# Kernel tuning notes

Measured on AMD Instinct MI355X. Metric: run time of the kernel, lower is better.

The kernel has to match this reference:

```python
import jax, jax.numpy as jnp
import numpy as np

_BASE = [[15,13],[13,11],[16,14],[14,12],[11,12],[5,11],[6,12],[5,6],[5,7],[6,8],[7,9],[8,10],[1,2],[0,1],[0,2],[1,3],[2,4],[3,5],[4,6]]
_CONN_NP = np.array(_BASE + [[b, a] for a, b in _BASE], dtype=np.int64).T  # [2, 38]: row0=src, row1=dst
N_NODES = 17
_ADJ_NP = np.zeros((N_NODES, N_NODES), dtype=bool)
_ADJ_NP[_CONN_NP[1], _CONN_NP[0]] = True   # message flows src -> dst: mask[dst, src]
np.fill_diagonal(_ADJ_NP, True)            # PyG GATConv add_self_loops=True default
ADJ = jnp.asarray(_ADJ_NP)
CONN = jnp.asarray(_CONN_NP)

B, T, NUM_CLASSES, HEADS = 128, 24, 500, 8
LSTM_H = 512
FEAT = N_NODES * 256 + 256  # 4608
NEG_INF = -1e9


def _gat_layer(x, W, a_src, a_dst, b, concat):
    # x: [G, 17, Cin]; W: [Cin, H*D]; a_src/a_dst: [H, D]; dense attention over tiny 17-node graph
    G, N, _ = x.shape
    H, D = a_src.shape
    h = (x @ W).reshape(G, N, H, D)
    s_src = jnp.einsum('gnhd,hd->gnh', h, a_src)
    s_dst = jnp.einsum('gnhd,hd->gnh', h, a_dst)
    e = jax.nn.leaky_relu(s_dst[:, :, None, :] + s_src[:, None, :, :], 0.2)  # [G, i_dst, j_src, H]
    e = jnp.where(ADJ[None, :, :, None], e, NEG_INF)
    alpha = jax.nn.softmax(e, axis=2)  # softmax over incoming neighbors j (incl. self loop)
    out = jnp.einsum('gijh,gjhd->gihd', alpha, h)
    out = out.reshape(G, N, H * D) if concat else out.mean(axis=2)
    return out + b


def _edge_feats(pose_flat):  # [G, 17, 3] -> [G, 38, 2] (bone lengths + angles)
    v = pose_flat[:, CONN[1], :2] - pose_flat[:, CONN[0], :2]
    lengths = jnp.linalg.norm(v, axis=-1)
    angles = jnp.arctan2(v[..., 1], v[..., 0])
    return jnp.stack([lengths, angles], axis=-1)


def _lstm_dir(x, Wih, Whh, bih, bhh):
    # x: [N, T, F] -> h sequence [N, T, H]; torch gate order i, f, g, o
    Hsz = Whh.shape[1]
    n = x.shape[0]
    def step(carry, xt):
        h, c = carry
        g = xt @ Wih.T + h @ Whh.T + bih + bhh
        i, f, gg, o = jnp.split(g, 4, axis=-1)
        c = jax.nn.sigmoid(f) * c + jax.nn.sigmoid(i) * jnp.tanh(gg)
        h = jax.nn.sigmoid(o) * jnp.tanh(c)
        return (h, c), h
    init = (jnp.zeros((n, Hsz), x.dtype), jnp.zeros((n, Hsz), x.dtype))
    _, hs = jax.lax.scan(step, init, jnp.swapaxes(x, 0, 1))
    return jnp.swapaxes(hs, 0, 1)


def _forward(pose1, pose2, W1, as1, ad1, b1, W2, as2, ad2, b2, W3, as3, ad3, b3,
             fc_w, fc_b, bn_g, bn_b, bn_mean, bn_var,
             Wih_f, Whh_f, bih_f, bhh_f, Wih_b, Whh_b, bih_b, bhh_b, cls_w, cls_b):
    def run(pose):
        x = pose.reshape(-1, N_NODES, 3)  # [B*T, 17, 3], all timestep graphs batched
        x = jax.nn.elu(_gat_layer(x, W1, as1, ad1, b1, True))   # [G,17,512]
        x = jax.nn.elu(_gat_layer(x, W2, as2, ad2, b2, True))   # [G,17,1024]
        x = _gat_layer(x, W3, as3, ad3, b3, False)              # [G,17,256]
        g = x.reshape(B, T, N_NODES * 256)
        ef = _edge_feats(pose.reshape(-1, N_NODES, 3)).reshape(-1, 38) @ fc_w + fc_b
        return jnp.concatenate([g, ef.reshape(B, T, -1)], axis=-1)  # [B,T,4608]
    comb = jnp.concatenate([run(pose1), run(pose2)], axis=0)  # modal==0 path: [2B,24,4608]
    # BatchNorm1d(24) in eval mode: normalize the time-channel axis with running stats
    comb = (comb - bn_mean[None, :, None]) * (bn_g[None, :, None] / jnp.sqrt(bn_var[None, :, None] + 1e-5)) + bn_b[None, :, None]
    hf = _lstm_dir(comb, Wih_f, Whh_f, bih_f, bhh_f)
    hb = jnp.flip(_lstm_dir(jnp.flip(comb, 1), Wih_b, Whh_b, bih_b, bhh_b), 1)
    lstm_out = jnp.concatenate([hf, hb], axis=-1)[:, -1, :]  # [2B, 1024]
    return lstm_out, lstm_out @ cls_w + cls_b


def setup_inputs():
    key = jax.random.key(0)
    ks = jax.random.split(key, 20)
    def w(k, shape):
        fan_in = shape[0] if len(shape) == 2 else shape[-1]
        return (jax.random.normal(k, shape, jnp.float32) / jnp.sqrt(jnp.float32(fan_in)))
    return {
        'pose1': jax.random.normal(ks[0], (B, T, N_NODES, 3), jnp.float32),
        'pose2': jax.random.normal(ks[1], (B, T, N_NODES, 3), jnp.float32),
        'modal': 0,
        'W1': w(ks[2], (3, HEADS * 64)), 'as1': w(ks[3], (HEADS, 64)), 'ad1': w(ks[4], (HEADS, 64)), 'b1': jnp.zeros((HEADS * 64,), jnp.float32),
        'W2': w(ks[5], (HEADS * 64, HEADS * 128)), 'as2': w(ks[6], (HEADS, 128)), 'ad2': w(ks[7], (HEADS, 128)), 'b2': jnp.zeros((HEADS * 128,), jnp.float32),
        'W3': w(ks[8], (HEADS * 128, HEADS * 256)), 'as3': w(ks[9], (HEADS, 256)), 'ad3': w(ks[10], (HEADS, 256)), 'b3': jnp.zeros((256,), jnp.float32),
        'fc_w': w(ks[11], (38, 128)), 'fc_b': jnp.zeros((128,), jnp.float32),
        'bn_g': jnp.ones((T,), jnp.float32), 'bn_b': jnp.zeros((T,), jnp.float32),
        'bn_mean': jnp.zeros((T,), jnp.float32), 'bn_var': jnp.ones((T,), jnp.float32),
        'Wih_f': w(ks[12], (4 * LSTM_H, FEAT)), 'Whh_f': w(ks[13], (4 * LSTM_H, LSTM_H)),
        'bih_f': jnp.zeros((4 * LSTM_H,), jnp.float32), 'bhh_f': jnp.zeros((4 * LSTM_H,), jnp.float32),
        'Wih_b': w(ks[14], (4 * LSTM_H, FEAT)), 'Whh_b': w(ks[15], (4 * LSTM_H, LSTM_H)),
        'bih_b': jnp.zeros((4 * LSTM_H,), jnp.float32), 'bhh_b': jnp.zeros((4 * LSTM_H,), jnp.float32),
        'cls_w': w(ks[16], (2 * LSTM_H, NUM_CLASSES)), 'cls_b': jnp.zeros((NUM_CLASSES,), jnp.float32),
    }


def reference(pose1, pose2, modal, W1, as1, ad1, b1, W2, as2, ad2, b2, W3, as3, ad3, b3,
              fc_w, fc_b, bn_g, bn_b, bn_mean, bn_var,
              Wih_f, Whh_f, bih_f, bhh_f, Wih_b, Whh_b, bih_b, bhh_b, cls_w, cls_b):
    # modal==0 path of the original forward (both modalities)
    return _forward(pose1, pose2, W1, as1, ad1, b1, W2, as2, ad2, b2, W3, as3, ad3, b3,
                    fc_w, fc_b, bn_g, bn_b, bn_mean, bn_var,
                    Wih_f, Whh_f, bih_f, bhh_f, Wih_b, Whh_b, bih_b, bhh_b, cls_w, cls_b)
```

## Files before the change

### kernel.cpp

```cpp
#include <hip/hip_runtime.h>
#include <hip/hip_bf16.h>

typedef __hip_bfloat16 bf16;
typedef short short8 __attribute__((ext_vector_type(8)));
typedef __bf16 bf16x8 __attribute__((ext_vector_type(8)));
typedef float f32x4 __attribute__((ext_vector_type(4)));
typedef const __attribute__((address_space(1))) void* gas_t;
typedef __attribute__((address_space(3))) void* las_t;

__constant__ unsigned int ADJM[17] = {
  0x00007u,0x0000Fu,0x00017u,0x0002Au,0x00054u,0x008E8u,0x01170u,0x002A0u,
  0x00540u,0x00280u,0x00500u,0x03820u,0x05840u,0x0A800u,0x15000u,0x0A000u,0x14000u};

__constant__ int EA[38] = {15,13,16,14,11,5,6,5,5,6,7,8,1,0,0,1,2,3,4,
                           13,11,14,12,12,11,12,6,7,8,9,10,2,1,2,3,4,5,6};
__constant__ int EB[38] = {13,11,14,12,12,11,12,6,7,8,9,10,2,1,2,3,4,5,6,
                           15,13,16,14,11,5,6,5,5,6,7,8,1,0,0,1,2,3,4};

__device__ __forceinline__ float b2f(bf16 v){ return __bfloat162float(v); }
__device__ __forceinline__ bf16 f2b(float v){ return __float2bfloat16(v); }
__device__ __forceinline__ float s2f(short s){
  unsigned u = ((unsigned)(unsigned short)s) << 16;
  float f; __builtin_memcpy(&f, &u, 4); return f;
}
__device__ __forceinline__ float ldx(const void* p, size_t i, int ext){
  return ext ? ((const float*)p)[i] : b2f(((const bf16*)p)[i]);
}
__device__ __forceinline__ void stx(void* p, size_t i, int ext, float v){
  if (ext) ((float*)p)[i] = v;
  else     ((bf16*)p)[i] = f2b(v);
}
__device__ __forceinline__ float sigm(float x){ return 1.f/(1.f + expf(-x)); }

__global__ void detect_k(const void* probe, int* flag){
  if (blockIdx.x == 0 && threadIdx.x == 0) {
    const bf16* p = (const bf16*)probe;
    int ext = 0;
    for (int i = 0; i < 256; i++) {
      float v = b2f(p[i]);
      if (!(fabsf(v) < 1e6f)) ext = 1;
    }
    *flag = ext;
  }
}

__global__ __launch_bounds__(256) void conv_k(
    const void* __restrict__ in, bf16* __restrict__ out, long n,
    const int* __restrict__ flg){
  int ext = *flg;
  long i = (long)blockIdx.x * 256 + threadIdx.x;
  if (i < n) out[i] = f2b(ldx(in, i, ext));
}

__global__ __launch_bounds__(256) void transp_k(
    const void* __restrict__ in, bf16* __restrict__ out, int K, int N,
    const int* __restrict__ flg){
  int ext = *flg;
  __shared__ float t[32][33];
  int k0 = blockIdx.y * 32, n0 = blockIdx.x * 32;
  int c = threadIdx.x & 31, r8 = threadIdx.x >> 5;
  for (int rr = r8; rr < 32; rr += 8) {
    int k = k0 + rr, n = n0 + c;
    t[rr][c] = (k < K && n < N) ? ldx(in, (size_t)k*N + n, ext) : 0.f;
  }
  __syncthreads();
  for (int rr = r8; rr < 32; rr += 8) {
    int n = n0 + rr, k = k0 + c;
    if (n < N && k < K) out[(size_t)n*K + k] = f2b(t[c][rr]);
  }
}

__global__ __launch_bounds__(256) void posepad_k(
    const void* __restrict__ pose1, const void* __restrict__ pose2,
    bf16* __restrict__ P32, const int* __restrict__ flg){
  int ext = *flg;
  long i = (long)blockIdx.x * 256 + threadIdx.x;
  if (i >= (long)6144*17*32) return;
  int col = i & 31; long rn = i >> 5;
  int n = (int)(rn % 17); long g = rn / 17;
  float v = 0.f;
  if (col < 3) {
    int pose = g >= 3072 ? 1 : 0;
    long gp = g - (pose ? 3072 : 0);
    v = ldx(pose ? pose2 : pose1, gp*51 + n*3 + col, ext);
  }
  P32[i] = f2b(v);
}

__global__ __launch_bounds__(256) void w1pad_k(
    const void* __restrict__ W1, bf16* __restrict__ W1p,
    const int* __restrict__ flg){
  int ext = *flg;
  int i = blockIdx.x * 256 + threadIdx.x;
  if (i >= 512*32) return;
  int col = i & 31, n = i >> 5;
  W1p[i] = f2b(col < 3 ? ldx(W1, (size_t)col*512 + n, ext) : 0.f);
}

__global__ __launch_bounds__(256) void smallprep_k(
    const void* s0, const void* s1, const void* s2, const void* s3,
    const void* s4, const void* s5, const void* s6, const void* s7,
    const void* s8, const void* s9, const void* s10,
    const void* bng, const void* bnb, const void* bnm, const void* bnv,
    bf16* __restrict__ sml, const int* __restrict__ flg)
{
  int ext = *flg;
  if (blockIdx.x == 55) {
    int t = threadIdx.x;
    if (t < 24) {
      float sc = ldx(bng, t, ext) * rsqrtf(ldx(bnv, t, ext) + 1e-5f);
      float sh = ldx(bnb, t, ext) - ldx(bnm, t, ext) * sc;
      sml[14080 + t] = f2b(sc);
      sml[14112 + t] = f2b(sh);
    }
    return;
  }
  long gidx = (long)blockIdx.x*256 + threadIdx.x;
  if (gidx >= 13952) return;
  const void* srcs[11] = {s0,s1,s2,s3,s4,s5,s6,s7,s8,s9,s10};
  const int lens[11] = {512,512,512,1024,1024,1024,2048,2048,256,4864,128};
  int seg = 0; long off = gidx;
  while (off >= lens[seg]) { off -= lens[seg]; seg++; }
  sml[gidx] = f2b(ldx(srcs[seg], off, ext));
}

__global__ __launch_bounds__(256) void gemm_mfma(
    const bf16* __restrict__ A, long lda,
    const bf16* __restrict__ Bt, long ldb,
    void* __restrict__ Cout, long ldc, int outF32,
    const float* __restrict__ addsrc, long ldadd,
    const void* __restrict__ bias0, const void* __restrict__ bias1,
    int M, int N, int K, const int* __restrict__ flg)
{
  __shared__ short lsA[128*32];
  __shared__ short lsB[128*32];
  int tid = threadIdx.x;
  int lane = tid & 63, w = tid >> 6;
  int wm = (w >> 1) * 64, wn = (w & 1) * 64;
  int lr = lane & 15;
  int lk = (lane >> 4) * 8;
  int m0 = blockIdx.y * 128, n0 = blockIdx.x * 128;
  const short* Ag = (const short*)A;
  const short* Bg = (const short*)Bt;
  int rowS = tid >> 2;
  int kqS  = (tid & 3) * 8;

  f32x4 acc[4][4];
#pragma unroll
  for (int i = 0; i < 4; i++)
#pragma unroll
    for (int j = 0; j < 4; j++) acc[i][j] = (f32x4)0.f;

  for (int kb = 0; kb < K; kb += 32) {
#pragma unroll
    for (int s = 0; s < 2; s++) {
      int row = s*64 + rowS;
      const short* ga = Ag + (size_t)(m0+row)*lda + kb + kqS;
      const short* gb = Bg + (size_t)(n0+row)*ldb + kb + kqS;
      __builtin_amdgcn_global_load_lds((gas_t)ga, (las_t)(lsA + s*2048 + w*512), 16, 0, 0);
      __builtin_amdgcn_global_load_lds((gas_t)gb, (las_t)(lsB + s*2048 + w*512), 16, 0, 0);
    }
    __syncthreads();
    bf16x8 af[4], bfr[4];
#pragma unroll
    for (int i = 0; i < 4; i++)
      af[i] = *(bf16x8*)&lsA[(wm + i*16 + lr)*32 + lk];
#pragma unroll
    for (int j = 0; j < 4; j++)
      bfr[j] = *(bf16x8*)&lsB[(wn + j*16 + lr)*32 + lk];
#pragma unroll
    for (int i = 0; i < 4; i++)
#pragma unroll
      for (int j = 0; j < 4; j++)
        acc[i][j] = __builtin_amdgcn_mfma_f32_16x16x32_bf16(af[i], bfr[j], acc[i][j], 0, 0, 0);
    __syncthreads();
  }

  int ext = flg ? *flg : 0;
#pragma unroll
  for (int j = 0; j < 4; j++) {
    int col = n0 + wn + j*16 + (lane & 15);
    float bsum = 0.f;
    if (bias0) bsum += ldx(bias0, col, ext);
    if (bias1) bsum += ldx(bias1, col, ext);
#pragma unroll
    for (int i = 0; i < 4; i++) {
      int rowb = m0 + wm + i*16 + (lane >> 4)*4;
#pragma unroll
      for (int r = 0; r < 4; r++) {
        float v = acc[i][j][r] + bsum;
        int row = rowb + r;
        if (addsrc) v += addsrc[(size_t)row*ldadd + col];
        size_t ci = (size_t)row*ldc + col;
        if (outF32) ((float*)Cout)[ci] = v;
        else        ((bf16*)Cout)[ci] = f2b(v);
      }
    }
  }
}

__global__ __launch_bounds__(256) void gemm_k(
    const void* __restrict__ A, long aOff, long lda, int aMode,
    const void* __restrict__ B, long ldb, int bT, int bExt,
    void* __restrict__ Cout, long outOff, long ldc, int outMode,
    const float* __restrict__ addsrc, long ldadd,
    const void* __restrict__ bias0, const void* __restrict__ bias1,
    int M, int N, int K, const int* __restrict__ flg)
{
  int ext  = *flg;
  int aF32 = (aMode == 1) || (aMode == 2 && ext);
  int bF32 = (bExt && ext);
  int oF32 = (outMode == 1) || (outMode == 2 && ext);

  __shared__ float As[16][64];
  __shared__ float Bs[16][64];
  int tid = threadIdx.x;
  int tx = tid & 15, ty = tid >> 4;
  int m0 = blockIdx.y * 64, n0 = blockIdx.x * 64;
  float acc[4][4] = {};

  for (int kb = 0; kb < K; kb += 16) {
#pragma unroll
    for (int i = 0; i < 4; i++) {
      int idx = i*256 + tid;
      int m = idx & 63, k = idx >> 6;
      int gm = m0 + m, gk = kb + k;
      float v = 0.f;
      if (gm < M && gk < K) {
        size_t ai = (size_t)aOff + (size_t)gm*lda + gk;
        v = aF32 ? ((const float*)A)[ai] : b2f(((const bf16*)A)[ai]);
      }
      As[k][m] = v;
    }
#pragma unroll
    for (int i = 0; i < 4; i++) {
      int idx = i*256 + tid;
      int n = idx & 63, k = idx >> 6;
      int gn = n0 + n, gk = kb + k;
      float v = 0.f;
      if (gn < N && gk < K) {
        size_t bi = bT ? (size_t)gn*ldb + gk : (size_t)gk*ldb + gn;
        v = bF32 ? ((const float*)B)[bi] : b2f(((const bf16*)B)[bi]);
      }
      Bs[k][n] = v;
    }
    __syncthreads();
#pragma unroll
    for (int kk = 0; kk < 16; kk++) {
      float a[4], b[4];
#pragma unroll
      for (int i = 0; i < 4; i++) a[i] = As[kk][ty*4 + i];
#pragma unroll
      for (int j = 0; j < 4; j++) b[j] = Bs[kk][tx*4 + j];
#pragma unroll
      for (int i = 0; i < 4; i++)
#pragma unroll
        for (int j = 0; j < 4; j++)
          acc[i][j] = fmaf(a[i], b[j], acc[i][j]);
    }
    __syncthreads();
  }

#pragma unroll
  for (int i = 0; i < 4; i++) {
    int gm = m0 + ty*4 + i;
    if (gm >= M) continue;
#pragma unroll
    for (int j = 0; j < 4; j++) {
      int gn = n0 + tx*4 + j;
      if (gn >= N) continue;
      float v = acc[i][j];
      if (bias0)  v += ldx(bias0, gn, ext);
      if (bias1)  v += ldx(bias1, gn, ext);
      if (addsrc) v += addsrc[(size_t)gm*ldadd + gn];
      size_t ci = (size_t)outOff + (size_t)gm*ldc + gn;
      if (oF32) ((float*)Cout)[ci] = v;
      else      ((bf16*)Cout)[ci] = f2b(v);
    }
  }
}

__global__ __launch_bounds__(256) void scoremax_k(
    const bf16* __restrict__ H,
    const bf16* __restrict__ aS, const bf16* __restrict__ aD,
    float* __restrict__ alphaG, int D, int HD)
{
  __shared__ float sS[17][8], sD_[17][8];
  int g = blockIdx.x, tid = threadIdx.x;
  int lane = tid & 63, w = tid >> 6;
  int cpl = HD >> 6;
  int col0 = lane * cpl;
  int h = lane >> 3;
  const short* Hgs = (const short*)(H + (size_t)g*17*HD);
  const short* a0 = (const short*)aS;
  const short* a1 = (const short*)aD;

  for (int n = w; n < 17; n += 4) {
    float s0 = 0.f, s1 = 0.f;
    const short* hp = Hgs + (size_t)n*HD + col0;
    for (int z = 0; z < cpl; z += 8) {
      short8 hv = *(const short8*)&hp[z];
      short8 v0 = *(const short8*)&a0[col0 + z];
      short8 v1 = *(const short8*)&a1[col0 + z];
#pragma unroll
      for (int e = 0; e < 8; e++) {
        float hf = s2f(hv[e]);
        s0 = fmaf(hf, s2f(v0[e]), s0);
        s1 = fmaf(hf, s2f(v1[e]), s1);
      }
    }
#pragma unroll
    for (int off = 1; off < 8; off <<= 1) {
      s0 += __shfl_xor(s0, off);
      s1 += __shfl_xor(s1, off);
    }
    if ((lane & 7) == 0) { sS[n][h] = s0; sD_[n][h] = s1; }
  }
  __syncthreads();

  if (tid < 136) {
    int i = tid >> 3, hh = tid & 7;
    unsigned int msk = ADJM[i];
    float e[17], m = -1e30f;
    for (int j = 0; j < 17; j++)
      if ((msk >> j) & 1u) {
        float v = sD_[i][hh] + sS[j][hh];
        v = v > 0.f ? v : 0.2f * v;
        e[j] = v;
        if (v > m) m = v;
      }
    float sum = 0.f;
    float wv[17];
    for (int j = 0; j < 17; j++) {
      float wj = 0.f;
      if ((msk >> j) & 1u) { wj = expf(e[j] - m); sum += wj; }
      wv[j] = wj;
    }
    float inv = 1.f / sum;
    float* ag = alphaG + (size_t)g*2312;
    for (int j = 0; j < 17; j++)
      ag[(i*17 + j)*8 + hh] = wv[j] * inv;
  }
}

__global__ __launch_bounds__(256) void agg_k(
    const bf16* __restrict__ H, const float* __restrict__ alphaG,
    const bf16* __restrict__ bias,
    bf16* __restrict__ Xout, bf16* __restrict__ comb,
    const bf16* __restrict__ bnsc_, const bf16* __restrict__ bnsh_,
    int D, int HD, int meanMode, int chunkStart)
{
  __shared__ float al[2312];
  int g = blockIdx.x, tid = threadIdx.x;
  for (int v = tid; v < 2312; v += 256) al[v] = alphaG[(size_t)g*2312 + v];
  __syncthreads();
  const short* Hgs = (const short*)(H + (size_t)g*17*HD);

  if (!meanMode) {
    int nc = HD >> 8;
    for (int cc = 0; cc < nc; cc++) {
      int c = cc*256 + tid;
      int h = c / D;
      float Hreg[17];
#pragma unroll
      for (int j = 0; j < 17; j++) Hreg[j] = s2f(Hgs[(size_t)j*HD + c]);
      float b0 = b2f(bias[c]);
      for (int i = 0; i < 17; i++) {
        float acc = b0;
#pragma unroll
        for (int j = 0; j < 17; j++)
          acc = fmaf(al[(i*17 + j)*8 + h], Hreg[j], acc);
        float v = acc > 0.f ? acc : expm1f(acc);
        Xout[((size_t)g*17 + i)*HD + c] = f2b(v);
      }
    }
  } else {
    float acc[17];
#pragma unroll
    for (int i = 0; i < 17; i++) acc[i] = 0.f;
    for (int hh = 0; hh < 8; hh++) {
      float Hreg[17];
#pragma unroll
      for (int j = 0; j < 17; j++)
        Hreg[j] = s2f(Hgs[(size_t)j*2048 + hh*256 + tid]);
      for (int i = 0; i < 17; i++) {
        float a = acc[i];
#pragma unroll
        for (int j = 0; j < 17; j++)
          a = fmaf(al[(i*17 + j)*8 + hh], Hreg[j], a);
        acc[i] = a;
      }
    }
    int gg = chunkStart + g;
    int pose = gg >= 3072 ? 1 : 0;
    int gp = gg - pose*3072;
    int bb = gp / 24, t = gp - bb*24;
    int r = (pose*128 + bb)*24 + t;
    float sc = b2f(bnsc_[t]);
    float sh = b2f(bnsh_[t]);
    float b0 = b2f(bias[tid]);
#pragma unroll
    for (int i = 0; i < 17; i++) {
      float v = acc[i] * 0.125f + b0;
      comb[(size_t)r*4608 + i*256 + tid] = f2b(v * sc + sh);
    }
  }
}

__global__ __launch_bounds__(256) void ef_k(
    const void* __restrict__ pose1, const void* __restrict__ pose2,
    const bf16* __restrict__ fcw, const bf16* __restrict__ fcb,
    bf16* __restrict__ comb,
    const bf16* __restrict__ bnsc_, const bf16* __restrict__ bnsh_,
    const int* __restrict__ flg)
{
  int ext = *flg;
  int g = blockIdx.x;
  int pose = g >= 3072 ? 1 : 0;
  int gp = g - pose*3072;
  const void* P = pose ? pose2 : pose1;
  size_t base = (size_t)gp * 51;
  __shared__ float feat[76];
  int tid = threadIdx.x;
  if (tid < 38) {
    int a = EA[tid], b = EB[tid];
    float ax = ldx(P, base + a*3+0, ext), ay = ldx(P, base + a*3+1, ext);
    float bx = ldx(P, base + b*3+0, ext), by = ldx(P, base + b*3+1, ext);
    float vx = bx - ax, vy = by - ay;
    feat[2*tid]   = sqrtf(vx*vx + vy*vy);
    feat[2*tid+1] = atan2f(vy, vx);
  }
  __syncthreads();
  int bb = gp / 24, t = gp - bb*24;
  int r = (pose*128 + bb)*24 + t;
  float sc = b2f(bnsc_[t]), sh = b2f(bnsh_[t]);
  int row = tid >> 7, c = tid & 127;
  float acc = b2f(fcb[c]);
  for (int k = 0; k < 38; k++)
    acc = fmaf(feat[row*38 + k], b2f(fcw[k*128 + c]), acc);
  comb[(size_t)r*4608 + 4352 + row*128 + c] = f2b(acc * sc + sh);
}

__global__ __launch_bounds__(256) void lstm_point(
    const float* __restrict__ gates, long gstride,
    const float* __restrict__ cprev,
    float* __restrict__ cout_, float* __restrict__ hout,
    bf16* __restrict__ h16,
    void* __restrict__ dout, float* __restrict__ fout, int doff,
    const int* __restrict__ flg)
{
  int ext = *flg;
  int idx = blockIdx.x * 256 + threadIdx.x;
  if (idx >= 256*512) return;
  int n = idx >> 9, u = idx & 511;
  const float* gp = gates + (size_t)n * gstride;
  float gi = gp[u], gf = gp[512+u], gc = gp[1024+u], go = gp[1536+u];
  float cp = cprev ? cprev[idx] : 0.f;
  float c = sigm(gf)*cp + sigm(gi)*tanhf(gc);
  float h = sigm(go)*tanhf(c);
  cout_[idx] = c;
  if (hout) hout[idx] = h;
  if (h16) h16[idx] = f2b(h);
  if (dout) stx(dout, (size_t)n*1024 + doff + u, ext, h);
  if (fout) fout[(size_t)n*1024 + doff + u] = h;
}

extern "C" void kernel_launch(void* const* d_in, const int* in_sizes, int n_in,
                              void* d_out, int out_size, void* d_ws, size_t ws_size,
                              hipStream_t stream)
{
  const void* pose1 = d_in[0];
  const void* pose2 = d_in[1];
  int wb = (n_in == 30) ? 2 : 3;
  const void* W1  = d_in[wb+0];
  const void* as1 = d_in[wb+1];
  const void* ad1 = d_in[wb+2];
  const void* b1  = d_in[wb+3];
  const void* W2  = d_in[wb+4];
  const void* as2 = d_in[wb+5];
  const void* ad2 = d_in[wb+6];
  const void* b2  = d_in[wb+7];
  const void* W3  = d_in[wb+8];
  const void* as3 = d_in[wb+9];
  const void* ad3 = d_in[wb+10];
  const void* b3  = d_in[wb+11];
  const void* fcw = d_in[wb+12];
  const void* fcb = d_in[wb+13];
  const void* bng = d_in[wb+14];
  const void* bnb = d_in[wb+15];
  const void* bnm = d_in[wb+16];
  const void* bnv = d_in[wb+17];
  const void* Wih_f = d_in[wb+18];
  const void* Whh_f = d_in[wb+19];
  const void* bih_f = d_in[wb+20];
  const void* bhh_f = d_in[wb+21];
  const void* Wih_b = d_in[wb+22];
  const void* Whh_b = d_in[wb+23];
  const void* bih_b = d_in[wb+24];
  const void* bhh_b = d_in[wb+25];
  const void* cls_w = d_in[wb+26];
  const void* cls_b = d_in[wb+27];
  (void)Whh_b;

  auto al = [](size_t x){ return (x + 255) & ~(size_t)255; };
  size_t flagB  = 256;
  size_t combB  = al((size_t)6144*4608*2);
  size_t gatesB_ = al((size_t)256*2048*4);
  size_t gatesBB = al((size_t)256*2048*4);
  size_t cB     = al((size_t)256*512*4);
  size_t h16B   = al((size_t)256*512*2);
  size_t l32B   = al((size_t)256*1024*4);
  size_t w2tB   = al((size_t)1024*512*2);
  size_t w3tB   = al((size_t)2048*1024*2);
  size_t whhB   = al((size_t)2048*512*2);
  size_t wihB   = al((size_t)2048*4608*2);
  size_t p32B   = al((size_t)6144*17*32*2);
  size_t w1pB   = al((size_t)512*32*2);
  size_t smlB   = al((size_t)32768*2);
  size_t xifB   = al((size_t)6144*2048*4);
  size_t fixB   = flagB + combB + gatesB_ + gatesBB + cB + h16B + l32B
                + w2tB + w3tB + whhB + 2*wihB + p32B + w1pB + smlB;
  auto chunkB = [&](int C){
    return al((size_t)C*17*2048*2) + al((size_t)C*17*1024*2)
         + al((size_t)C*2312*4);
  };
  const int cands[8] = {3072,1536,768,384,192,96,48,24};
  int CHUNK = 0; bool useXIf = false;
  for (int i = 0; i < 8 && !CHUNK; i++)
    if (fixB + xifB + chunkB(cands[i]) <= ws_size) { CHUNK = cands[i]; useXIf = true; }
  for (int i = 0; i < 8 && !CHUNK; i++)
    if (fixB + chunkB(cands[i]) <= ws_size) CHUNK = cands[i];
  if (!CHUNK) CHUNK = 24;

  char* ws = (char*)d_ws;
  size_t off = 0;
  auto alloc = [&](size_t bytes) -> void* { void* p = ws + off; off += bytes; return p; };
  int*   dflag  = (int*)  alloc(flagB);
  bf16*  comb   = (bf16*) alloc(combB);
  float* gates  = (float*)alloc(gatesB_);
  float* gatesBw= (float*)alloc(gatesBB);
  float* cbuf   = (float*)alloc(cB);
  bf16*  h16    = (bf16*) alloc(h16B);
  float* lstm32 = (float*)alloc(l32B);
  bf16*  W2t    = (bf16*) alloc(w2tB);
  bf16*  W3t    = (bf16*) alloc(w3tB);
  bf16*  WhhC   = (bf16*) alloc(whhB);
  bf16*  WihfC  = (bf16*) alloc(wihB);
  bf16*  WihbC  = (bf16*) alloc(wihB);
  bf16*  P32    = (bf16*) alloc(p32B);
  bf16*  W1p    = (bf16*) alloc(w1pB);
  bf16*  sml    = (bf16*) alloc(smlB);
  float* XIf    = useXIf ? (float*)alloc(xifB) : nullptr;
  bf16*  Hbuf   = (bf16*) alloc(al((size_t)CHUNK*17*2048*2));
  bf16*  Xbuf   = (bf16*) alloc(al((size_t)CHUNK*17*1024*2));
  float* alphaA = (float*)alloc(al((size_t)CHUNK*2312*4));

  bf16* as1c = sml;          bf16* ad1c = sml + 512;
  bf16* b1c  = sml + 1024;   bf16* as2c = sml + 1536;
  bf16* ad2c = sml + 2560;   bf16* b2c  = sml + 3584;
  bf16* as3c = sml + 4608;   bf16* ad3c = sml + 6656;
  bf16* b3c  = sml + 8704;   bf16* fcwc = sml + 8960;
  bf16* fcbc = sml + 13824;  bf16* bnsc = sml + 14080;
  bf16* bnsh = sml + 14112;

  int RPC = CHUNK * 17;
  int gy  = (RPC + 63) / 64;
  int nchunks = 6144 / CHUNK;
  bool mfmaGat = (RPC % 128) == 0;
  dim3 blk(256);

  detect_k<<<dim3(1), dim3(64), 0, stream>>>(pose1, dflag);

  long nWih = (long)2048*4608;
  conv_k<<<dim3((unsigned)((nWih+255)/256)), blk, 0, stream>>>(Wih_f, WihfC, nWih, dflag);
  conv_k<<<dim3((unsigned)((nWih+255)/256)), blk, 0, stream>>>(Wih_b, WihbC, nWih, dflag);
  long nWhh = (long)2048*512;
  conv_k<<<dim3((unsigned)((nWhh+255)/256)), blk, 0, stream>>>(Whh_f, WhhC, nWhh, dflag);
  transp_k<<<dim3(1024/32, 512/32), blk, 0, stream>>>(W2, W2t, 512, 1024, dflag);
  transp_k<<<dim3(2048/32, 1024/32), blk, 0, stream>>>(W3, W3t, 1024, 2048, dflag);
  posepad_k<<<dim3((unsigned)(((long)6144*17*32+255)/256)), blk, 0, stream>>>(pose1, pose2, P32, dflag);
  w1pad_k<<<dim3(64), blk, 0, stream>>>(W1, W1p, dflag);
  smallprep_k<<<dim3(56), blk, 0, stream>>>(
      as1, ad1, b1, as2, ad2, b2, as3, ad3, b3, fcw, fcb,
      bng, bnb, bnm, bnv, sml, dflag);

  for (int c = 0; c < nchunks; c++) {
    int cstart = c * CHUNK;
    if (mfmaGat)
      gemm_mfma<<<dim3(512/128, RPC/128), blk, 0, stream>>>(
          P32 + (size_t)cstart*17*32, 32L, W1p, 32L, Hbuf, 512L, 0,
          (const float*)nullptr, 0L, nullptr, nullptr, RPC, 512, 32, dflag);
    else {
      int pose   = cstart / 3072;
      long pOff  = (long)(cstart % 3072) * 51;
      gemm_k<<<dim3(512/64, gy), blk, 0, stream>>>(
          pose ? pose2 : pose1, pOff, 3L, 2, W1, 512L, 0, 1, Hbuf, 0L, 512L, 0,
          (const float*)nullptr, 0L, (const void*)nullptr, (const void*)nullptr,
          RPC, 512, 3, dflag);
    }
    scoremax_k<<<dim3(CHUNK), blk, 0, stream>>>(Hbuf, as1c, ad1c, alphaA, 64, 512);
    agg_k<<<dim3(CHUNK), blk, 0, stream>>>(
        Hbuf, alphaA, b1c, Xbuf, (bf16*)nullptr,
        (const bf16*)nullptr, (const bf16*)nullptr, 64, 512, 0, 0);
    if (mfmaGat)
      gemm_mfma<<<dim3(1024/128, RPC/128), blk, 0, stream>>>(
          Xbuf, 512L, W2t, 512L, Hbuf, 1024L, 0,
          (const float*)nullptr, 0L, nullptr, nullptr, RPC, 1024, 512, dflag);
    else
      gemm_k<<<dim3(1024/64, gy), blk, 0, stream>>>(
          Xbuf, 0L, 512L, 0, W2t, 512L, 1, 0, Hbuf, 0L, 1024L, 0,
          (const float*)nullptr, 0L, (const void*)nullptr, (const void*)nullptr,
          RPC, 1024, 512, dflag);
    scoremax_k<<<dim3(CHUNK), blk, 0, stream>>>(Hbuf, as2c, ad2c, alphaA, 128, 1024);
    agg_k<<<dim3(CHUNK), blk, 0, stream>>>(
        Hbuf, alphaA, b2c, Xbuf, (bf16*)nullptr,
        (const bf16*)nullptr, (const bf16*)nullptr, 128, 1024, 0, 0);
    if (mfmaGat)
      gemm_mfma<<<dim3(2048/128, RPC/128), blk, 0, stream>>>(
          Xbuf, 1024L, W3t, 1024L, Hbuf, 2048L, 0,
          (const float*)nullptr, 0L, nullptr, nullptr, RPC, 2048, 1024, dflag);
    else
      gemm_k<<<dim3(2048/64, gy), blk, 0, stream>>>(
          Xbuf, 0L, 1024L, 0, W3t, 1024L, 1, 0, Hbuf, 0L, 2048L, 0,
          (const float*)nullptr, 0L, (const void*)nullptr, (const void*)nullptr,
          RPC, 2048, 1024, dflag);
    scoremax_k<<<dim3(CHUNK), blk, 0, stream>>>(Hbuf, as3c, ad3c, alphaA, 256, 2048);
    agg_k<<<dim3(CHUNK), blk, 0, stream>>>(
        Hbuf, alphaA, b3c, (bf16*)nullptr, comb,
        bnsc, bnsh, 256, 2048, 1, cstart);
  }

  ef_k<<<dim3(6144), blk, 0, stream>>>(pose1, pose2, fcwc, fcbc, comb,
                                       bnsc, bnsh, dflag);

  gemm_mfma<<<dim3(2048/128, 256/128), blk, 0, stream>>>(
      comb + (size_t)23*4608, (long)24*4608, WihbC, 4608L, gatesBw, 2048L, 1,
      (const float*)nullptr, 0L, bih_b, bhh_b, 256, 2048, 4608, dflag);

  if (useXIf) {
    gemm_mfma<<<dim3(2048/128, 6144/128), blk, 0, stream>>>(
        comb, 4608L, WihfC, 4608L, XIf, 2048L, 1,
        (const float*)nullptr, 0L, bih_f, bhh_f, 6144, 2048, 4608, dflag);
    lstm_point<<<dim3(512), blk, 0, stream>>>(
        XIf, (long)24*2048, (const float*)nullptr, cbuf, (float*)nullptr, h16,
        (void*)nullptr, (float*)nullptr, 0, dflag);
    for (int t = 1; t < 24; t++) {
      gemm_mfma<<<dim3(2048/128, 256/128), blk, 0, stream>>>(
          h16, 512L, WhhC, 512L, gates, 2048L, 1,
          XIf + (size_t)t*2048, (long)24*2048,
          nullptr, nullptr, 256, 2048, 512, dflag);
      lstm_point<<<dim3(512), blk, 0, stream>>>(
          gates, 2048L, cbuf, cbuf, (float*)nullptr, h16,
          (t == 23) ? d_out : (void*)nullptr,
          (t == 23) ? lstm32 : (float*)nullptr, 0, dflag);
    }
  } else {
    for (int t = 0; t < 24; t++) {
      gemm_mfma<<<dim3(2048/128, 256/128), blk, 0, stream>>>(
          comb + (size_t)t*4608, (long)24*4608, WihfC, 4608L, gates, 2048L, 1,
          (const float*)nullptr, 0L, bih_f, bhh_f, 256, 2048, 4608, dflag);
      if (t > 0)
        gemm_mfma<<<dim3(2048/128, 256/128), blk, 0, stream>>>(
            h16, 512L, WhhC, 512L, gates, 2048L, 1,
            gates, 2048L, nullptr, nullptr, 256, 2048, 512, dflag);
      lstm_point<<<dim3(512), blk, 0, stream>>>(
          gates, 2048L, (t == 0) ? (const float*)nullptr : cbuf, cbuf,
          (float*)nullptr, h16,
          (t == 23) ? d_out : (void*)nullptr,
          (t == 23) ? lstm32 : (float*)nullptr, 0, dflag);
    }
  }

  lstm_point<<<dim3(512), blk, 0, stream>>>(
      gatesBw, 2048L, (const float*)nullptr, cbuf, (float*)nullptr,
      (bf16*)nullptr, d_out, lstm32, 512, dflag);

  gemm_k<<<dim3((500+63)/64, 256/64), blk, 0, stream>>>(
      lstm32, 0L, 1024L, 1, cls_w, 500L, 0, 1, d_out, 262144L, 500L, 2,
      (const float*)nullptr, 0L, cls_b, (const void*)nullptr, 256, 500, 1024, dflag);
}
```

Measured before the change: 3.562 ms.

## Fuse GAT score/aggregate kernels and LSTM recurrent GEMM with pointwise update

Merges the GAT attention-score and aggregation kernels into one kernel that keeps the attention weights in shared memory, removing the global alpha buffer round trip and one launch per layer. The LSTM weights are reordered so the four gates of each unit sit next to each other. That lets a new per-step kernel do the h·Whh MFMA and the cell update together, with ping-pong h buffers and pre-summed biases. This halves launches in the 24-step recurrence and removes the gates round trip through global memory. The cost is a small 64x64 tile grid (128 blocks) for the recurrent GEMM, which may leave much of the GPU idle.

After: 2.993 ms. 1.19x faster.

```diff
diff --git a/kernel.cpp b/kernel.cpp
--- a/kernel.cpp
+++ b/kernel.cpp
@@ -44,12 +44,27 @@
   }
 }
 
-__global__ __launch_bounds__(256) void conv_k(
-    const void* __restrict__ in, bf16* __restrict__ out, long n,
+__global__ __launch_bounds__(256) void reord_k(
+    const void* __restrict__ in, bf16* __restrict__ out, int K,
     const int* __restrict__ flg){
   int ext = *flg;
   long i = (long)blockIdx.x * 256 + threadIdx.x;
-  if (i < n) out[i] = f2b(ldx(in, i, ext));
+  if (i >= (long)2048*K) return;
+  long rowp = i / K, k = i - rowp*K;
+  int u = (int)(rowp >> 2), g = (int)(rowp & 3);
+  out[i] = f2b(ldx(in, (size_t)(g*512 + u)*K + k, ext));
+}
+
+__global__ __launch_bounds__(256) void biasprep_k(
+    const void* bihf, const void* bhhf, const void* bihb, const void* bhhb,
+    float* __restrict__ bIf, float* __restrict__ bIb,
+    const int* __restrict__ flg){
+  int ext = *flg;
+  int c = blockIdx.x*256 + threadIdx.x;
+  if (c >= 2048) return;
+  int u = c >> 2, g = c & 3;
+  bIf[c] = ldx(bihf, (size_t)g*512+u, ext) + ldx(bhhf, (size_t)g*512+u, ext);
+  bIb[c] = ldx(bihb, (size_t)g*512+u, ext) + ldx(bhhb, (size_t)g*512+u, ext);
 }
 
 __global__ __launch_bounds__(256) void transp_k(
@@ -280,41 +295,47 @@
   }
 }
 
-__global__ __launch_bounds__(256) void scoremax_k(
+__global__ __launch_bounds__(256) void attn_k(
     const bf16* __restrict__ H,
     const bf16* __restrict__ aS, const bf16* __restrict__ aD,
-    float* __restrict__ alphaG, int D, int HD)
+    const bf16* __restrict__ bias,
+    bf16* __restrict__ Xout, bf16* __restrict__ comb,
+    const bf16* __restrict__ bnsc_, const bf16* __restrict__ bnsh_,
+    int D, int HD, int meanMode, int chunkStart)
 {
   __shared__ float sS[17][8], sD_[17][8];
+  __shared__ float al[2312];
   int g = blockIdx.x, tid = threadIdx.x;
   int lane = tid & 63, w = tid >> 6;
-  int cpl = HD >> 6;
-  int col0 = lane * cpl;
-  int h = lane >> 3;
   const short* Hgs = (const short*)(H + (size_t)g*17*HD);
-  const short* a0 = (const short*)aS;
-  const short* a1 = (const short*)aD;
-
-  for (int n = w; n < 17; n += 4) {
-    float s0 = 0.f, s1 = 0.f;
-    const short* hp = Hgs + (size_t)n*HD + col0;
-    for (int z = 0; z < cpl; z += 8) {
-      short8 hv = *(const short8*)&hp[z];
-      short8 v0 = *(const short8*)&a0[col0 + z];
-      short8 v1 = *(const short8*)&a1[col0 + z];
-#pragma unroll
-      for (int e = 0; e < 8; e++) {
-        float hf = s2f(hv[e]);
-        s0 = fmaf(hf, s2f(v0[e]), s0);
-        s1 = fmaf(hf, s2f(v1[e]), s1);
-      }
-    }
-#pragma unroll
-    for (int off = 1; off < 8; off <<= 1) {
-      s0 += __shfl_xor(s0, off);
-      s1 += __shfl_xor(s1, off);
-    }
-    if ((lane & 7) == 0) { sS[n][h] = s0; sD_[n][h] = s1; }
+
+  {
+    int cpl = HD >> 6;
+    int col0 = lane * cpl;
+    int h = lane >> 3;
+    const short* a0 = (const short*)aS;
+    const short* a1 = (const short*)aD;
+    for (int n = w; n < 17; n += 4) {
+      float s0 = 0.f, s1 = 0.f;
+      const short* hp = Hgs + (size_t)n*HD + col0;
+      for (int z = 0; z < cpl; z += 8) {
+        short8 hv = *(const short8*)&hp[z];
+        short8 v0 = *(const short8*)&a0[col0 + z];
+        short8 v1 = *(const short8*)&a1[col0 + z];
+#pragma unroll
+        for (int e = 0; e < 8; e++) {
+          float hf = s2f(hv[e]);
+          s0 = fmaf(hf, s2f(v0[e]), s0);
+          s1 = fmaf(hf, s2f(v1[e]), s1);
+        }
+      }
+#pragma unroll
+      for (int off = 1; off < 8; off <<= 1) {
+        s0 += __shfl_xor(s0, off);
+        s1 += __shfl_xor(s1, off);
+      }
+      if ((lane & 7) == 0) { sS[n][h] = s0; sD_[n][h] = s1; }
+    }
   }
   __syncthreads();
 
@@ -329,32 +350,16 @@
         e[j] = v;
         if (v > m) m = v;
       }
-    float sum = 0.f;
-    float wv[17];
+    float sum = 0.f, wv[17];
     for (int j = 0; j < 17; j++) {
       float wj = 0.f;
       if ((msk >> j) & 1u) { wj = expf(e[j] - m); sum += wj; }
       wv[j] = wj;
     }
     float inv = 1.f / sum;
-    float* ag = alphaG + (size_t)g*2312;
-    for (int j = 0; j < 17; j++)
-      ag[(i*17 + j)*8 + hh] = wv[j] * inv;
-  }
-}
-
-__global__ __launch_bounds__(256) void agg_k(
-    const bf16* __restrict__ H, const float* __restrict__ alphaG,
-    const bf16* __restrict__ bias,
-    bf16* __restrict__ Xout, bf16* __restrict__ comb,
-    const bf16* __restrict__ bnsc_, const bf16* __restrict__ bnsh_,
-    int D, int HD, int meanMode, int chunkStart)
-{
-  __shared__ float al[2312];
-  int g = blockIdx.x, tid = threadIdx.x;
-  for (int v = tid; v < 2312; v += 256) al[v] = alphaG[(size_t)g*2312 + v];
+    for (int j = 0; j < 17; j++) al[(i*17 + j)*8 + hh] = wv[j] * inv;
+  }
   __syncthreads();
-  const short* Hgs = (const short*)(H + (size_t)g*17*HD);
 
   if (!meanMode) {
     int nc = HD >> 8;
@@ -441,28 +446,95 @@
   comb[(size_t)r*4608 + 4352 + row*128 + c] = f2b(acc * sc + sh);
 }
 
-__global__ __launch_bounds__(256) void lstm_point(
-    const float* __restrict__ gates, long gstride,
-    const float* __restrict__ cprev,
-    float* __restrict__ cout_, float* __restrict__ hout,
-    bf16* __restrict__ h16,
-    void* __restrict__ dout, float* __restrict__ fout, int doff,
+__global__ __launch_bounds__(256) void lstm_step_k(
+    const bf16* __restrict__ WhhI, const float* __restrict__ XI,
+    long xstride, long xoff,
+    const bf16* __restrict__ hin, bf16* __restrict__ hout,
+    float* __restrict__ cbuf, int useC,
+    float* __restrict__ lstm32, void* __restrict__ dout, int isLast,
     const int* __restrict__ flg)
 {
-  int ext = *flg;
-  int idx = blockIdx.x * 256 + threadIdx.x;
+  __shared__ short lsA[64*32];
+  __shared__ short lsB[64*32];
+  __shared__ float gbuf[64*64];
+  int tid = threadIdx.x;
+  int lane = tid & 63, w = tid >> 6;
+  int lr = lane & 15, lk = (lane >> 4)*8;
+  int rowS = tid >> 2, kqS = (tid & 3)*8;
+  int n0 = blockIdx.y * 64, c0 = blockIdx.x * 64;
+
+  f32x4 acc[4];
+#pragma unroll
+  for (int j = 0; j < 4; j++) acc[j] = (f32x4)0.f;
+
+  if (useC) {
+    const short* Ag = (const short*)hin;
+    const short* Bg = (const short*)WhhI;
+    for (int kb = 0; kb < 512; kb += 32) {
+      __builtin_amdgcn_global_load_lds((gas_t)(Ag + (size_t)(n0+rowS)*512 + kb + kqS),
+                                       (las_t)(lsA + w*512), 16, 0, 0);
+      __builtin_amdgcn_global_load_lds((gas_t)(Bg + (size_t)(c0+rowS)*512 + kb + kqS),
+                                       (las_t)(lsB + w*512), 16, 0, 0);
+      __syncthreads();
+      bf16x8 af = *(bf16x8*)&lsA[(w*16 + lr)*32 + lk];
+#pragma unroll
+      for (int j = 0; j < 4; j++) {
+        bf16x8 bfr = *(bf16x8*)&lsB[(j*16 + lr)*32 + lk];
+        acc[j] = __builtin_amdgcn_mfma_f32_16x16x32_bf16(af, bfr, acc[j], 0, 0, 0);
+      }
+      __syncthreads();
+    }
+  }
+
+  int rowb = w*16 + (lane >> 4)*4;
+#pragma unroll
+  for (int j = 0; j < 4; j++) {
+    int lc = j*16 + lr;
+#pragma unroll
+    for (int r = 0; r < 4; r++) {
+      int lrow = rowb + r;
+      gbuf[lrow*64 + lc] =
+          acc[j][r] + XI[(size_t)(n0 + lrow)*xstride + xoff + c0 + lc];
+    }
+  }
+  __syncthreads();
+
+  int ext = *flg;
+#pragma unroll
+  for (int k = 0; k < 4; k++) {
+    int idx = tid*4 + k;
+    int lrow = idx >> 4, ul = idx & 15;
+    float gi = gbuf[lrow*64 + ul*4 + 0];
+    float gf = gbuf[lrow*64 + ul*4 + 1];
+    float gg = gbuf[lrow*64 + ul*4 + 2];
+    float go = gbuf[lrow*64 + ul*4 + 3];
+    int n = n0 + lrow;
+    int u = (c0 >> 2) + ul;
+    float cp = useC ? cbuf[(size_t)n*512 + u] : 0.f;
+    float c = sigm(gf)*cp + sigm(gi)*tanhf(gg);
+    float h = sigm(go)*tanhf(c);
+    cbuf[(size_t)n*512 + u] = c;
+    hout[(size_t)n*512 + u] = f2b(h);
+    if (isLast) {
+      lstm32[(size_t)n*1024 + u] = h;
+      stx(dout, (size_t)n*1024 + u, ext, h);
+    }
+  }
+}
+
+__global__ __launch_bounds__(256) void lstm_bwd_k(
+    const float* __restrict__ gB, float* __restrict__ lstm32,
+    void* __restrict__ dout, const int* __restrict__ flg)
+{
+  int ext = *flg;
+  int idx = blockIdx.x*256 + threadIdx.x;
   if (idx >= 256*512) return;
   int n = idx >> 9, u = idx & 511;
-  const float* gp = gates + (size_t)n * gstride;
-  float gi = gp[u], gf = gp[512+u], gc = gp[1024+u], go = gp[1536+u];
-  float cp = cprev ? cprev[idx] : 0.f;
-  float c = sigm(gf)*cp + sigm(gi)*tanhf(gc);
-  float h = sigm(go)*tanhf(c);
-  cout_[idx] = c;
-  if (hout) hout[idx] = h;
-  if (h16) h16[idx] = f2b(h);
-  if (dout) stx(dout, (size_t)n*1024 + doff + u, ext, h);
-  if (fout) fout[(size_t)n*1024 + doff + u] = h;
+  const float* gp = gB + (size_t)n*2048 + u*4;
+  float c = sigm(gp[0])*tanhf(gp[2]);
+  float h = sigm(gp[3])*tanhf(c);
+  lstm32[(size_t)n*1024 + 512 + u] = h;
+  stx(dout, (size_t)n*1024 + 512 + u, ext, h);
 }
 
 extern "C" void kernel_launch(void* const* d_in, const int* in_sizes, int n_in,
@@ -510,6 +582,7 @@
   size_t cB     = al((size_t)256*512*4);
   size_t h16B   = al((size_t)256*512*2);
   size_t l32B   = al((size_t)256*1024*4);
+  size_t bIB    = al((size_t)2048*4);
   size_t w2tB   = al((size_t)1024*512*2);
   size_t w3tB   = al((size_t)2048*1024*2);
   size_t whhB   = al((size_t)2048*512*2);
@@ -518,11 +591,10 @@
   size_t w1pB   = al((size_t)512*32*2);
   size_t smlB   = al((size_t)32768*2);
   size_t xifB   = al((size_t)6144*2048*4);
-  size_t fixB   = flagB + combB + gatesB_ + gatesBB + cB + h16B + l32B
-                + w2tB + w3tB + whhB + 2*wihB + p32B + w1pB + smlB;
+  size_t fixB   = flagB + combB + gatesB_ + gatesBB + cB + 2*h16B + l32B
+                + 2*bIB + w2tB + w3tB + whhB + 2*wihB + p32B + w1pB + smlB;
   auto chunkB = [&](int C){
-    return al((size_t)C*17*2048*2) + al((size_t)C*17*1024*2)
-         + al((size_t)C*2312*4);
+    return al((size_t)C*17*2048*2) + al((size_t)C*17*1024*2);
   };
   const int cands[8] = {3072,1536,768,384,192,96,48,24};
   int CHUNK = 0; bool useXIf = false;
@@ -540,20 +612,23 @@
   float* gates  = (float*)alloc(gatesB_);
   float* gatesBw= (float*)alloc(gatesBB);
   float* cbuf   = (float*)alloc(cB);
-  bf16*  h16    = (bf16*) alloc(h16B);
+  bf16*  h16a   = (bf16*) alloc(h16B);
+  bf16*  h16b   = (bf16*) alloc(h16B);
   float* lstm32 = (float*)alloc(l32B);
+  float* biasIf = (float*)alloc(bIB);
+  float* biasIb = (float*)alloc(bIB);
   bf16*  W2t    = (bf16*) alloc(w2tB);
   bf16*  W3t    = (bf16*) alloc(w3tB);
-  bf16*  WhhC   = (bf16*) alloc(whhB);
-  bf16*  WihfC  = (bf16*) alloc(wihB);
-  bf16*  WihbC  = (bf16*) alloc(wihB);
+  bf16*  WhhI   = (bf16*) alloc(whhB);
+  bf16*  WihfI  = (bf16*) alloc(wihB);
+  bf16*  WihbI  = (bf16*) alloc(wihB);
   bf16*  P32    = (bf16*) alloc(p32B);
   bf16*  W1p    = (bf16*) alloc(w1pB);
   bf16*  sml    = (bf16*) alloc(smlB);
   float* XIf    = useXIf ? (float*)alloc(xifB) : nullptr;
   bf16*  Hbuf   = (bf16*) alloc(al((size_t)CHUNK*17*2048*2));
   bf16*  Xbuf   = (bf16*) alloc(al((size_t)CHUNK*17*1024*2));
-  float* alphaA = (float*)alloc(al((size_t)CHUNK*2312*4));
+  bf16*  hbufs[2] = {h16a, h16b};
 
   bf16* as1c = sml;          bf16* ad1c = sml + 512;
   bf16* b1c  = sml + 1024;   bf16* as2c = sml + 1536;
@@ -572,10 +647,12 @@
   detect_k<<<dim3(1), dim3(64), 0, stream>>>(pose1, dflag);
 
   long nWih = (long)2048*4608;
-  conv_k<<<dim3((unsigned)((nWih+255)/256)), blk, 0, stream>>>(Wih_f, WihfC, nWih, dflag);
-  conv_k<<<dim3((unsigned)((nWih+255)/256)), blk, 0, stream>>>(Wih_b, WihbC, nWih, dflag);
+  reord_k<<<dim3((unsigned)((nWih+255)/256)), blk, 0, stream>>>(Wih_f, WihfI, 4608, dflag);
+  reord_k<<<dim3((unsigned)((nWih+255)/256)), blk, 0, stream>>>(Wih_b, WihbI, 4608, dflag);
   long nWhh = (long)2048*512;
-  conv_k<<<dim3((unsigned)((nWhh+255)/256)), blk, 0, stream>>>(Whh_f, WhhC, nWhh, dflag);
+  reord_k<<<dim3((unsigned)((nWhh+255)/256)), blk, 0, stream>>>(Whh_f, WhhI, 512, dflag);
+  biasprep_k<<<dim3(8), blk, 0, stream>>>(bih_f, bhh_f, bih_b, bhh_b,
+                                          biasIf, biasIb, dflag);
   transp_k<<<dim3(1024/32, 512/32), blk, 0, stream>>>(W2, W2t, 512, 1024, dflag);
   transp_k<<<dim3(2048/32, 1024/32), blk, 0, stream>>>(W3, W3t, 1024, 2048, dflag);
   posepad_k<<<dim3((unsigned)(((long)6144*17*32+255)/256)), blk, 0, stream>>>(pose1, pose2, P32, dflag);
@@ -598,9 +675,8 @@
           (const float*)nullptr, 0L, (const void*)nullptr, (const void*)nullptr,
           RPC, 512, 3, dflag);
     }
-    scoremax_k<<<dim3(CHUNK), blk, 0, stream>>>(Hbuf, as1c, ad1c, alphaA, 64, 512);
-    agg_k<<<dim3(CHUNK), blk, 0, stream>>>(
-        Hbuf, alphaA, b1c, Xbuf, (bf16*)nullptr,
+    attn_k<<<dim3(CHUNK), blk, 0, stream>>>(
+        Hbuf, as1c, ad1c, b1c, Xbuf, (bf16*)nullptr,
         (const bf16*)nullptr, (const bf16*)nullptr, 64, 512, 0, 0);
     if (mfmaGat)
       gemm_mfma<<<dim3(1024/128, RPC/128), blk, 0, stream>>>(
@@ -611,9 +687,8 @@
           Xbuf, 0L, 512L, 0, W2t, 512L, 1, 0, Hbuf, 0L, 1024L, 0,
           (const float*)nullptr, 0L, (const void*)nullptr, (const void*)nullptr,
           RPC, 1024, 512, dflag);
-    scoremax_k<<<dim3(CHUNK), blk, 0, stream>>>(Hbuf, as2c, ad2c, alphaA, 128, 1024);
-    agg_k<<<dim3(CHUNK), blk, 0, stream>>>(
-        Hbuf, alphaA, b2c, Xbuf, (bf16*)nullptr,
+    attn_k<<<dim3(CHUNK), blk, 0, stream>>>(
+        Hbuf, as2c, ad2c, b2c, Xbuf, (bf16*)nullptr,
         (const bf16*)nullptr, (const bf16*)nullptr, 128, 1024, 0, 0);
     if (mfmaGat)
       gemm_mfma<<<dim3(2048/128, RPC/128), blk, 0, stream>>>(
@@ -624,9 +699,8 @@
           Xbuf, 0L, 1024L, 0, W3t, 1024L, 1, 0, Hbuf, 0L, 2048L, 0,
           (const float*)nullptr, 0L, (const void*)nullptr, (const void*)nullptr,
           RPC, 2048, 1024, dflag);
-    scoremax_k<<<dim3(CHUNK), blk, 0, stream>>>(Hbuf, as3c, ad3c, alphaA, 256, 2048);
-    agg_k<<<dim3(CHUNK), blk, 0, stream>>>(
-        Hbuf, alphaA, b3c, (bf16*)nullptr, comb,
+    attn_k<<<dim3(CHUNK), blk, 0, stream>>>(
+        Hbuf, as3c, ad3c, b3c, (bf16*)nullptr, comb,
         bnsc, bnsh, 256, 2048, 1, cstart);
   }
 
@@ -634,46 +708,32 @@
                                        bnsc, bnsh, dflag);
 
   gemm_mfma<<<dim3(2048/128, 256/128), blk, 0, stream>>>(
-      comb + (size_t)23*4608, (long)24*4608, WihbC, 4608L, gatesBw, 2048L, 1,
-      (const float*)nullptr, 0L, bih_b, bhh_b, 256, 2048, 4608, dflag);
+      comb + (size_t)23*4608, (long)24*4608, WihbI, 4608L, gatesBw, 2048L, 1,
+      biasIb, 0L, nullptr, nullptr, 256, 2048, 4608, dflag);
 
   if (useXIf) {
     gemm_mfma<<<dim3(2048/128, 6144/128), blk, 0, stream>>>(
-        comb, 4608L, WihfC, 4608L, XIf, 2048L, 1,
-        (const float*)nullptr, 0L, bih_f, bhh_f, 6144, 2048, 4608, dflag);
-    lstm_point<<<dim3(512), blk, 0, stream>>>(
-        XIf, (long)24*2048, (const float*)nullptr, cbuf, (float*)nullptr, h16,
-        (void*)nullptr, (float*)nullptr, 0, dflag);
-    for (int t = 1; t < 24; t++) {
-      gemm_mfma<<<dim3(2048/128, 256/128), blk, 0, stream>>>(
-          h16, 512L, WhhC, 512L, gates, 2048L, 1,
-          XIf + (size_t)t*2048, (long)24*2048,
-          nullptr, nullptr, 256, 2048, 512, dflag);
-      lstm_point<<<dim3(512), blk, 0, stream>>>(
-          gates, 2048L, cbuf, cbuf, (float*)nullptr, h16,
-          (t == 23) ? d_out : (void*)nullptr,
-          (t == 23) ? lstm32 : (float*)nullptr, 0, dflag);
+        comb, 4608L, WihfI, 4608L, XIf, 2048L, 1,
+        biasIf, 0L, nullptr, nullptr, 6144, 2048, 4608, dflag);
+    for (int t = 0; t < 24; t++) {
+      lstm_step_k<<<dim3(32, 4), blk, 0, stream>>>(
+          WhhI, XIf, (long)24*2048, (long)t*2048,
+          hbufs[t & 1], hbufs[(t + 1) & 1], cbuf, (t > 0) ? 1 : 0,
+          lstm32, d_out, (t == 23) ? 1 : 0, dflag);
     }
   } else {
     for (int t = 0; t < 24; t++) {
       gemm_mfma<<<dim3(2048/128, 256/128), blk, 0, stream>>>(
-          comb + (size_t)t*4608, (long)24*4608, WihfC, 4608L, gates, 2048L, 1,
-          (const float*)nullptr, 0L, bih_f, bhh_f, 256, 2048, 4608, dflag);
-      if (t > 0)
-        gemm_mfma<<<dim3(2048/128, 256/128), blk, 0, stream>>>(
-            h16, 512L, WhhC, 512L, gates, 2048L, 1,
-            gates, 2048L, nullptr, nullptr, 256, 2048, 512, dflag);
-      lstm_point<<<dim3(512), blk, 0, stream>>>(
-          gates, 2048L, (t == 0) ? (const float*)nullptr : cbuf, cbuf,
-          (float*)nullptr, h16,
-          (t == 23) ? d_out : (void*)nullptr,
-          (t == 23) ? lstm32 : (float*)nullptr, 0, dflag);
-    }
-  }
-
-  lstm_point<<<dim3(512), blk, 0, stream>>>(
-      gatesBw, 2048L, (const float*)nullptr, cbuf, (float*)nullptr,
-      (bf16*)nullptr, d_out, lstm32, 512, dflag);
+          comb + (size_t)t*4608, (long)24*4608, WihfI, 4608L, gates, 2048L, 1,
+          biasIf, 0L, nullptr, nullptr, 256, 2048, 4608, dflag);
+      lstm_step_k<<<dim3(32, 4), blk, 0, stream>>>(
+          WhhI, gates, 2048L, 0L,
+          hbufs[t & 1], hbufs[(t + 1) & 1], cbuf, (t > 0) ? 1 : 0,
+          lstm32, d_out, (t == 23) ? 1 : 0, dflag);
+    }
+  }
+
+  lstm_bwd_k<<<dim3(512), blk, 0, stream>>>(gatesBw, lstm32, d_out, dflag);
 
   gemm_k<<<dim3((500+63)/64, 256/64), blk, 0, stream>>>(
       lstm32, 0L, 1024L, 1, cls_w, 500L, 0, 1, d_out, 262144L, 500L, 2,
```
